# Performance work log

Measured on AMD Instinct MI355X. Metric: run time of the kernel, lower is better.

Reference implementation:

```python
import jax, jax.numpy as jnp
import numpy as np

EPS = 1e-6
NEG_SLOPE = 0.01  # torch LeakyReLU default

def ln(x, g, b):
    m = jnp.mean(x, axis=-1, keepdims=True)
    v = jnp.mean((x - m) ** 2, axis=-1, keepdims=True)
    return (x - m) / jnp.sqrt(v + EPS) * g + b

def leaky(x):
    return jnp.where(x >= 0, x, NEG_SLOPE * x)

def setup_inputs() -> dict:
    B, L, F, H, NH, LBL = 8, 1024, 1024, 256, 8, 4766
    key = jax.random.key(0)
    ks = jax.random.split(key, 16)
    def lin(k, i, o, s=0.03):
        kw, kb = jax.random.split(k)
        return jax.random.normal(kw, (i, o), jnp.float32) * s, jnp.zeros((o,), jnp.float32)
    w_in, b_in = lin(ks[0], F, H)
    w_h, b_h = lin(ks[1], H, H)
    a_w1, a_b1 = lin(ks[2], H, 64)
    a_w2, a_b2 = lin(ks[3], 64, NH)
    o_w1, o_b1 = lin(ks[4], NH * H, NH * H)
    o_w2, o_b2 = lin(ks[5], NH * H, LBL)
    CM = (jax.random.uniform(ks[6], (LBL, LBL)) < 0.002).astype(jnp.float32)
    CM = jnp.maximum(CM, jnp.eye(LBL, dtype=jnp.float32))
    return {
        'h_V': jax.random.normal(ks[7], (B, L, F), jnp.float32),
        'mask': jnp.ones((B, L), jnp.int32),
        'ln0_g': jnp.ones((F,), jnp.float32), 'ln0_b': jnp.zeros((F,), jnp.float32),
        'w_in': w_in, 'b_in': b_in,
        'ln1_g': jnp.ones((H,), jnp.float32), 'ln1_b': jnp.zeros((H,), jnp.float32),
        'w_h': w_h, 'b_h': b_h,
        'ln2_g': jnp.ones((H,), jnp.float32), 'ln2_b': jnp.zeros((H,), jnp.float32),
        'a_w1': a_w1, 'a_b1': a_b1,
        'a_lng': jnp.ones((64,), jnp.float32), 'a_lnb': jnp.zeros((64,), jnp.float32),
        'a_w2': a_w2, 'a_b2': a_b2,
        'o_w1': o_w1, 'o_b1': o_b1,
        'o_lng': jnp.ones((NH * H,), jnp.float32), 'o_lnb': jnp.zeros((NH * H,), jnp.float32),
        'o_w2': o_w2, 'o_b2': o_b2,
        'CM': CM,
    }

def reference(h_V, mask, ln0_g, ln0_b, w_in, b_in, ln1_g, ln1_b, w_h, b_h,
              ln2_g, ln2_b, a_w1, a_b1, a_lng, a_lnb, a_w2, a_b2,
              o_w1, o_b1, o_lng, o_lnb, o_w2, o_b2, CM):
    B = h_V.shape[0]
    # input + hidden blocks (eval mode: dropout is identity)
    x = ln(h_V, ln0_g, ln0_b)
    x = leaky(x @ w_in + b_in)
    x = ln(x, ln1_g, ln1_b)
    x = leaky(x @ w_h + b_h)
    x = ln(x, ln2_g, ln2_b)                      # [B,L,H]
    # multi-head attention pooling over sequence
    a = leaky(x @ a_w1 + a_b1)
    a = ln(a, a_lng, a_lnb)
    a = a @ a_w2 + a_b2                          # [B,L,NH]
    a = jnp.where(mask[:, :, None] == 0, jnp.float32(-1e9), a)
    a = jax.nn.softmax(a, axis=1)
    h = jnp.einsum('blh,bld->bhd', a, x).reshape(B, -1)  # [B,NH*H]
    # output block
    h = leaky(h @ o_w1 + o_b1)
    h = ln(h, o_lng, o_lnb)
    p = jax.nn.sigmoid(h @ o_w2 + o_b2)          # [B,LBL]
    # GO-hierarchy max-product propagation (eval path)
    out = jnp.max(p[:, None, :] * CM[None, :, :], axis=-1)  # [B,LBL]
    return out.astype(jnp.float32)
```

## Files before the change

### kernel.cpp

```cpp
#include <hip/hip_runtime.h>
#include <hip/hip_bf16.h>
#include <cstdint>

#define B_   8
#define L_   1024
#define F_   1024
#define H_   256
#define NH_  8
#define LBL_ 4766
#define M_   (B_*L_)
#define OD_  (NH_*H_)
#define NCM  (LBL_*LBL_)
#define MP_EPB 16384
#define MP_NB  ((NCM + MP_EPB - 1) / MP_EPB)

typedef unsigned short u16;
typedef unsigned int   u32;
typedef __attribute__((ext_vector_type(8))) short short8;
typedef __attribute__((ext_vector_type(4))) float float4v;

#define BF16_ONES_PAIR 0x3f803f80u

__device__ __forceinline__ float bf2f(u32 u) { return __uint_as_float(u << 16); }
__device__ __forceinline__ u16 f2bf(float f) {
    u32 u = __float_as_uint(f);
    u32 r = 0x7fffu + ((u >> 16) & 1u);
    return (u16)((u + r) >> 16);
}

struct f8 { float v[8]; };

__device__ __forceinline__ float ldS(const void* p, size_t i, bool bf) {
    return bf ? bf2f(((const u16*)p)[i]) : ((const float*)p)[i];
}
__device__ __forceinline__ float4 ld4(const void* p, size_t i, bool bf) {
    if (bf) {
        uint2 u = *(const uint2*)((const u16*)p + i);
        return make_float4(bf2f(u.x & 0xffff), bf2f(u.x >> 16),
                           bf2f(u.y & 0xffff), bf2f(u.y >> 16));
    }
    return *(const float4*)((const float*)p + i);
}
__device__ __forceinline__ f8 ld8(const void* p, size_t i, bool bf) {
    f8 r;
    if (bf) {
        uint4 u = *(const uint4*)((const u16*)p + i);
        r.v[0]=bf2f(u.x&0xffff); r.v[1]=bf2f(u.x>>16);
        r.v[2]=bf2f(u.y&0xffff); r.v[3]=bf2f(u.y>>16);
        r.v[4]=bf2f(u.z&0xffff); r.v[5]=bf2f(u.z>>16);
        r.v[6]=bf2f(u.w&0xffff); r.v[7]=bf2f(u.w>>16);
    } else {
        const float* q = (const float*)p + i;
        float4 a = *(const float4*)q, b = *(const float4*)(q+4);
        r.v[0]=a.x; r.v[1]=a.y; r.v[2]=a.z; r.v[3]=a.w;
        r.v[4]=b.x; r.v[5]=b.y; r.v[6]=b.z; r.v[7]=b.w;
    }
    return r;
}

__device__ __forceinline__ float wave_sum(float v) {
    #pragma unroll
    for (int m = 1; m < 64; m <<= 1) v += __shfl_xor(v, m, 64);
    return v;
}
__device__ __forceinline__ float wave_max(float v) {
    #pragma unroll
    for (int m = 1; m < 64; m <<= 1) v = fmaxf(v, __shfl_xor(v, m, 64));
    return v;
}
__device__ __forceinline__ float blk_sum(float v, float* sh) {
    v = wave_sum(v);
    int w = threadIdx.x >> 6, nw = blockDim.x >> 6;
    if ((threadIdx.x & 63) == 0) sh[w] = v;
    __syncthreads();
    float s = sh[0];
    for (int i = 1; i < nw; ++i) s += sh[i];
    __syncthreads();
    return s;
}
__device__ __forceinline__ float blk_max(float v, float* sh) {
    v = wave_max(v);
    int w = threadIdx.x >> 6, nw = blockDim.x >> 6;
    if ((threadIdx.x & 63) == 0) sh[w] = v;
    __syncthreads();
    float s = sh[0];
    for (int i = 1; i < nw; ++i) s = fmaxf(s, sh[i]);
    __syncthreads();
    return s;
}

__global__ __launch_bounds__(256) void transw_k(const void* __restrict__ W,
        u16* __restrict__ WT, int K, int N, const u32* __restrict__ probe) {
    __shared__ u16 tile[64][65];
    bool bf = (probe[0] == BF16_ONES_PAIR);
    int t = threadIdx.x;
    int kt = blockIdx.x * 64, nt = blockIdx.y * 64;
    int r = t >> 2, cq = (t & 3) * 16;
    #pragma unroll
    for (int j = 0; j < 4; ++j) {
        float4 v = ld4(W, (size_t)(kt + r) * N + nt + cq + j * 4, bf);
        tile[r][cq + j*4 + 0] = f2bf(v.x);
        tile[r][cq + j*4 + 1] = f2bf(v.y);
        tile[r][cq + j*4 + 2] = f2bf(v.z);
        tile[r][cq + j*4 + 3] = f2bf(v.w);
    }
    __syncthreads();
    #pragma unroll
    for (int j = 0; j < 4; ++j) {
        int k = cq + j * 4;
        u32 a0 = tile[k+0][r], a1 = tile[k+1][r], a2 = tile[k+2][r], a3 = tile[k+3][r];
        uint2 o; o.x = a0 | (a1 << 16); o.y = a2 | (a3 << 16);
        *(uint2*)(WT + (size_t)(nt + r) * K + kt + k) = o;
    }
}

__global__ __launch_bounds__(256) void lnwrite_k(const void* __restrict__ hv,
        const void* __restrict__ g, const void* __restrict__ b,
        u16* __restrict__ x0, const u32* __restrict__ probe) {
    __shared__ float sh[4];
    bool bf = (probe[0] == BF16_ONES_PAIR);
    int row = blockIdx.x, t = threadIdx.x;
    float4 v = ld4(hv, (size_t)row * F_ + t * 4, bf);
    float s = v.x + v.y + v.z + v.w;
    float q = v.x*v.x + v.y*v.y + v.z*v.z + v.w*v.w;
    s = blk_sum(s, sh);
    q = blk_sum(q, sh);
    float mean = s * (1.f / F_);
    float rstd = rsqrtf(q * (1.f / F_) - mean * mean + 1e-6f);
    float4 gg = ld4(g, t * 4, bf);
    float4 bb = ld4(b, t * 4, bf);
    u32 o0 = f2bf((v.x - mean) * rstd * gg.x + bb.x)
           | ((u32)f2bf((v.y - mean) * rstd * gg.y + bb.y) << 16);
    u32 o1 = f2bf((v.z - mean) * rstd * gg.z + bb.z)
           | ((u32)f2bf((v.w - mean) * rstd * gg.w + bb.w) << 16);
    *(uint2*)(x0 + (size_t)row * F_ + t * 4) = make_uint2(o0, o1);
}

__global__ __launch_bounds__(64) void rowstats_bf_k(const u16* __restrict__ x,
        float2* __restrict__ stat) {
    int row = blockIdx.x, t = threadIdx.x;
    uint2 u = ((const uint2*)(x + (size_t)row * 256))[t];
    float a0 = bf2f(u.x & 0xffff), a1 = bf2f(u.x >> 16);
    float a2 = bf2f(u.y & 0xffff), a3 = bf2f(u.y >> 16);
    float s = wave_sum(a0 + a1 + a2 + a3);
    float q = wave_sum(a0*a0 + a1*a1 + a2*a2 + a3*a3);
    if (t == 0) {
        float m = s * (1.f / 256), v = q * (1.f / 256) - m * m;
        stat[row] = make_float2(m, rsqrtf(v + 1e-6f));
    }
}

__global__ __launch_bounds__(256) void gemm_mfma(const u16* __restrict__ Ap, int amode,
        const float2* __restrict__ stat, const void* __restrict__ g,
        const void* __restrict__ bta, const u16* __restrict__ WT,
        const void* __restrict__ bias, u16* __restrict__ C, int M, int N, int K,
        const u32* __restrict__ probe) {
    __shared__ short8 As[64][5];
    __shared__ short8 Bs[64][5];
    bool pbf = (probe[0] == BF16_ONES_PAIR);
    int t = threadIdx.x;
    int m0 = blockIdx.x * 64, n0 = blockIdx.y * 64;
    int r = t >> 2, kq = t & 3;
    int l = t & 63, w = t >> 6;
    int q = l >> 4, ml = l & 15;
    float4v acc[4];
    #pragma unroll
    for (int nt = 0; nt < 4; ++nt)
        #pragma unroll
        for (int i = 0; i < 4; ++i) acc[nt][i] = 0.f;
    float2 st = (amode == 1) ? stat[m0 + r] : make_float2(0.f, 1.f);
    for (int k0 = 0; k0 < K; k0 += 32) {
        int kk = k0 + kq * 8;
        short8 pa;
        if (amode == 1) {
            f8 a  = ld8(Ap, (size_t)(m0 + r) * K + kk, true);
            f8 gg = ld8(g, kk, pbf);
            f8 bb = ld8(bta, kk, pbf);
            #pragma unroll
            for (int j = 0; j < 8; ++j)
                pa[j] = (short)f2bf((a.v[j] - st.x) * st.y * gg.v[j] + bb.v[j]);
        } else {
            pa = *(const short8*)(Ap + (size_t)(m0 + r) * K + kk);
        }
        short8 pb = *(const short8*)(WT + (size_t)(n0 + r) * K + kk);
        __syncthreads();
        As[r][kq] = pa;
        Bs[r][kq] = pb;
        __syncthreads();
        short8 af = As[w * 16 + ml][q];
        #pragma unroll
        for (int nt = 0; nt < 4; ++nt)
            acc[nt] = __builtin_amdgcn_mfma_f32_16x16x32_bf16(af, Bs[nt*16 + ml][q],
                                                              acc[nt], 0, 0, 0);
    }
    #pragma unroll
    for (int nt = 0; nt < 4; ++nt) {
        int nn = n0 + nt * 16 + ml;
        float bv = ldS(bias, nn, pbf);
        #pragma unroll
        for (int reg = 0; reg < 4; ++reg) {
            float v = acc[nt][reg] + bv;
            v = v >= 0.f ? v : 0.01f * v;
            C[(size_t)(m0 + w * 16 + q * 4 + reg) * N + nn] = f2bf(v);
        }
    }
}

__global__ __launch_bounds__(256) void attnlog_k(const u16* __restrict__ abr,
        const void* __restrict__ g, const void* __restrict__ b,
        const void* __restrict__ w2, const void* __restrict__ b2,
        const int* __restrict__ mask, float* __restrict__ lg,
        const u32* __restrict__ probe) {
    __shared__ float w2s[512];
    __shared__ float b2s[8];
    bool pbf = (probe[0] == BF16_ONES_PAIR);
    int t = threadIdx.x;
    for (int i = t; i < 512; i += 256) w2s[i] = ldS(w2, i, pbf);
    if (t < 8) b2s[t] = ldS(b2, t, pbf);
    __syncthreads();
    int l = t & 63, w = t >> 6;
    int row = blockIdx.x * 4 + w;
    float a = bf2f(abr[(size_t)row * 64 + l]);
    float s = wave_sum(a);
    float q = wave_sum(a * a);
    float m = s * (1.f / 64), var = q * (1.f / 64) - m * m;
    float val = (a - m) * rsqrtf(var + 1e-6f) * ldS(g, l, pbf) + ldS(b, l, pbf);
    float mine = 0.f;
    #pragma unroll
    for (int h = 0; h < 8; ++h) {
        float sh_ = wave_sum(val * w2s[l * 8 + h]);
        if (l == h) mine = sh_;
    }
    if (l < 8) {
        int bb = row >> 10, ll = row & 1023;
        float v = mine + b2s[l];
        if (mask[row] == 0) v = -1e9f;
        lg[((size_t)bb * NH_ + l) * L_ + ll] = v;
    }
}

__global__ __launch_bounds__(256) void softmax2_k(float* __restrict__ lg,
        const float2* __restrict__ st2, float* __restrict__ c1) {
    __shared__ float sh[4];
    int bh = blockIdx.x, t = threadIdx.x;
    int b = bh >> 3;
    size_t base = (size_t)bh * L_;
    float4 v = ((float4*)(lg + base))[t];
    float mx = blk_max(fmaxf(fmaxf(v.x, v.y), fmaxf(v.z, v.w)), sh);
    v.x = expf(v.x - mx); v.y = expf(v.y - mx);
    v.z = expf(v.z - mx); v.w = expf(v.w - mx);
    float s = blk_sum(v.x + v.y + v.z + v.w, sh);
    float inv = 1.f / s;
    float2 s0 = st2[(b << 10) + t*4 + 0];
    float2 s1 = st2[(b << 10) + t*4 + 1];
    float2 s2 = st2[(b << 10) + t*4 + 2];
    float2 s3 = st2[(b << 10) + t*4 + 3];
    float a0 = v.x * inv * s0.y, a1 = v.y * inv * s1.y;
    float a2 = v.z * inv * s2.y, a3 = v.w * inv * s3.y;
    ((float4*)(lg + base))[t] = make_float4(a0, a1, a2, a3);
    float c = blk_sum(a0 * s0.x + a1 * s1.x + a2 * s2.x + a3 * s3.x, sh);
    if (t == 0) c1[bh] = c;
}

__global__ __launch_bounds__(256) void pool_part_k(const float* __restrict__ lg,
        const u16* __restrict__ x2, float* __restrict__ Sp) {
    int bh = blockIdx.x, c = blockIdx.y, t = threadIdx.x;
    int b = bh >> 3, l0 = c << 8;
    const float* aw = lg + (size_t)bh * L_ + l0;
    const u16* xb = x2 + ((size_t)(b << 10) + l0) * 256;
    float acc = 0.f;
    #pragma unroll 4
    for (int i = 0; i < 256; ++i)
        acc += aw[i] * bf2f(xb[(size_t)i * 256 + t]);
    Sp[((size_t)c * 64 + bh) * 256 + t] = acc;
}

__global__ __launch_bounds__(256) void pool_comb_k(const float* __restrict__ Sp,
        const float* __restrict__ c1, const void* __restrict__ g,
        const void* __restrict__ b, float* __restrict__ hp,
        const u32* __restrict__ probe) {
    bool pbf = (probe[0] == BF16_ONES_PAIR);
    int bh = blockIdx.x, t = threadIdx.x;
    float S = Sp[(size_t)bh*256 + t] + Sp[(size_t)(64+bh)*256 + t]
            + Sp[(size_t)(128+bh)*256 + t] + Sp[(size_t)(192+bh)*256 + t];
    hp[(size_t)bh*256 + t] = (S - c1[bh]) * ldS(g, t, pbf) + ldS(b, t, pbf);
}

__global__ __launch_bounds__(256) void gemv2_k(const float* __restrict__ hv,
        const void* __restrict__ W, float* __restrict__ acc, int K, int N,
        const u32* __restrict__ probe) {
    __shared__ float hs[8 * 64];
    bool bf = (probe[0] == BF16_ONES_PAIR);
    int t = threadIdx.x;
    int kb = blockIdx.y * 64;
    for (int i = t; i < 512; i += 256) {
        int r = i >> 6, k = i & 63;
        hs[i] = hv[(size_t)r * K + kb + k];
    }
    __syncthreads();
    int c0 = (blockIdx.x * 256 + t) * 2;
    if (c0 >= N) return;
    float a[8][2] = {};
    #pragma unroll 4
    for (int k = 0; k < 64; ++k) {
        float w0, w1;
        if (bf) {
            u32 u = *(const u32*)((const u16*)W + (size_t)(kb + k) * N + c0);
            w0 = bf2f(u & 0xffff); w1 = bf2f(u >> 16);
        } else {
            float2 fw = *(const float2*)((const float*)W + (size_t)(kb + k) * N + c0);
            w0 = fw.x; w1 = fw.y;
        }
        #pragma unroll
        for (int r = 0; r < 8; ++r) {
            float h = hs[(r << 6) + k];
            a[r][0] += h * w0; a[r][1] += h * w1;
        }
    }
    bool ok1 = (c0 + 1 < N);
    #pragma unroll
    for (int r = 0; r < 8; ++r) {
        atomicAdd(&acc[(size_t)r * N + c0], a[r][0]);
        if (ok1) atomicAdd(&acc[(size_t)r * N + c0 + 1], a[r][1]);
    }
}

__global__ __launch_bounds__(256) void out_ln_k(float* __restrict__ h,
        const void* __restrict__ bias, const void* __restrict__ g,
        const void* __restrict__ b, const u32* __restrict__ probe) {
    __shared__ float sh[4];
    bool bf = (probe[0] == BF16_ONES_PAIR);
    int row = blockIdx.x, t = threadIdx.x;
    float v[8];
    float s = 0.f, q = 0.f;
    #pragma unroll
    for (int i = 0; i < 8; ++i) {
        int c = t + i * 256;
        float x = h[(size_t)row * OD_ + c] + ldS(bias, c, bf);
        x = x >= 0.f ? x : 0.01f * x;
        v[i] = x; s += x; q += x * x;
    }
    s = blk_sum(s, sh) * (1.f / OD_);
    q = blk_sum(q, sh) * (1.f / OD_);
    float rstd = rsqrtf(q - s * s + 1e-6f);
    #pragma unroll
    for (int i = 0; i < 8; ++i) {
        int c = t + i * 256;
        h[(size_t)row * OD_ + c] = (v[i] - s) * rstd * ldS(g, c, bf) + ldS(b, c, bf);
    }
}

__global__ __launch_bounds__(256) void sigmoid_t_k(const float* __restrict__ acc,
        const void* __restrict__ bias, float* __restrict__ pt,
        const u32* __restrict__ probe) {
    bool bf = (probe[0] == BF16_ONES_PAIR);
    int c = blockIdx.x * 256 + threadIdx.x;
    if (c >= LBL_) return;
    float bv = ldS(bias, c, bf);
    float o[8];
    #pragma unroll
    for (int r = 0; r < 8; ++r) {
        float v = acc[(size_t)r * LBL_ + c] + bv;
        o[r] = 1.f / (1.f + expf(-v));
    }
    float4* dst = (float4*)(pt + (size_t)c * 8);
    dst[0] = make_float4(o[0], o[1], o[2], o[3]);
    dst[1] = make_float4(o[4], o[5], o[6], o[7]);
}

__device__ __forceinline__ void mp_hit(u32 idx, float cmv,
        const float* __restrict__ pt, int* smax, u32 rowBase) {
    u32 i = idx / LBL_;
    u32 j = idx - i * LBL_;
    const float4* pj = (const float4*)(pt + (size_t)j * 8);
    float4 pa = pj[0], pb = pj[1];
    int base = (int)(i - rowBase) * 8;
    atomicMax(&smax[base + 0], __float_as_int(pa.x * cmv));
    atomicMax(&smax[base + 1], __float_as_int(pa.y * cmv));
    atomicMax(&smax[base + 2], __float_as_int(pa.z * cmv));
    atomicMax(&smax[base + 3], __float_as_int(pa.w * cmv));
    atomicMax(&smax[base + 4], __float_as_int(pb.x * cmv));
    atomicMax(&smax[base + 5], __float_as_int(pb.y * cmv));
    atomicMax(&smax[base + 6], __float_as_int(pb.z * cmv));
    atomicMax(&smax[base + 7], __float_as_int(pb.w * cmv));
}

__global__ __launch_bounds__(256) void maxprod3_k(const float* __restrict__ pt,
        const void* __restrict__ CM, float* __restrict__ out,
        const u32* __restrict__ probe) {
    __shared__ int smax[6 * 8];
    bool bf = (probe[0] == BF16_ONES_PAIR);
    int t = threadIdx.x;
    size_t blockStart = (size_t)blockIdx.x * MP_EPB;
    u32 rowBase = (u32)(blockStart / LBL_);
    for (int i = t; i < 48; i += 256) smax[i] = 0;
    __syncthreads();
    if (bf) {
        const u16* cm = (const u16*)CM;
        uint4 ch[8];
        size_t i0[8];
        #pragma unroll
        for (int u = 0; u < 8; ++u) {
            size_t idx0 = blockStart + ((size_t)u * 256 + t) * 8;
            i0[u] = idx0;
            ch[u] = (idx0 + 8 <= NCM) ? *(const uint4*)(cm + idx0)
                                      : make_uint4(0, 0, 0, 0);
        }
        #pragma unroll
        for (int u = 0; u < 8; ++u) {
            size_t idx0 = i0[u];
            if (idx0 + 8 <= NCM) {
                uint4 c4 = ch[u];
                if ((c4.x | c4.y | c4.z | c4.w) == 0) continue;
                u32 hw[4] = {c4.x, c4.y, c4.z, c4.w};
                #pragma unroll
                for (int d = 0; d < 4; ++d) {
                    u32 lo = hw[d] & 0xffff, hi = hw[d] >> 16;
                    if (lo) mp_hit((u32)idx0 + d*2,     bf2f(lo), pt, smax, rowBase);
                    if (hi) mp_hit((u32)idx0 + d*2 + 1, bf2f(hi), pt, smax, rowBase);
                }
            } else if (idx0 < NCM) {
                for (u32 e = 0; e < (u32)(NCM - idx0); ++e) {
                    u16 h = cm[idx0 + e];
                    if (h) mp_hit((u32)idx0 + e, bf2f(h), pt, smax, rowBase);
                }
            }
        }
    } else {
        const float* cm = (const float*)CM;
        #pragma unroll
        for (int u = 0; u < 16; ++u) {
            size_t idx0 = blockStart + ((size_t)u * 256 + t) * 4;
            if (idx0 >= NCM) continue;
            float v[4];
            if (idx0 + 4 <= NCM) {
                float4 f = *(const float4*)(cm + idx0);
                v[0] = f.x; v[1] = f.y; v[2] = f.z; v[3] = f.w;
            } else {
                v[0] = v[1] = v[2] = v[3] = 0.f;
                for (u32 e = 0; e < (u32)(NCM - idx0); ++e) v[e] = cm[idx0 + e];
            }
            if (v[0] == 0.f && v[1] == 0.f && v[2] == 0.f && v[3] == 0.f) continue;
            #pragma unroll
            for (int e = 0; e < 4; ++e)
                if (v[e] != 0.f) mp_hit((u32)idx0 + e, v[e], pt, smax, rowBase);
        }
    }
    __syncthreads();
    size_t lastIdx = blockStart + MP_EPB - 1;
    if (lastIdx >= NCM) lastIdx = NCM - 1;
    int nrows = (int)((u32)(lastIdx / LBL_) - rowBase) + 1;
    for (int s = t; s < nrows * 8; s += 256) {
        int v = smax[s];
        if (v != 0) {
            int rr = s >> 3, b = s & 7;
            atomicMax((int*)(out + (size_t)b * LBL_ + rowBase + rr), v);
        }
    }
}

extern "C" void kernel_launch(void* const* d_in, const int* in_sizes, int n_in,
                              void* d_out, int out_size, void* d_ws, size_t ws_size,
                              hipStream_t stream) {
    const void* hv   = d_in[0];
    const int* mask  = (const int*)d_in[1];
    const void* ln0g = d_in[2];
    const void* ln0b = d_in[3];
    const void* w_in = d_in[4];
    const void* b_in = d_in[5];
    const void* ln1g = d_in[6];
    const void* ln1b = d_in[7];
    const void* w_h  = d_in[8];
    const void* b_h  = d_in[9];
    const void* ln2g = d_in[10];
    const void* ln2b = d_in[11];
    const void* aw1  = d_in[12];
    const void* ab1  = d_in[13];
    const void* alng = d_in[14];
    const void* alnb = d_in[15];
    const void* aw2  = d_in[16];
    const void* ab2  = d_in[17];
    const void* ow1  = d_in[18];
    const void* ob1  = d_in[19];
    const void* olng = d_in[20];
    const void* olnb = d_in[21];
    const void* ow2  = d_in[22];
    const void* ob2  = d_in[23];
    const void* CM   = d_in[24];
    const u32* probe = (const u32*)ln0g;
    float* out = (float*)d_out;

    float* f = (float*)d_ws;
    float2* st1 = (float2*)f;
    float2* st2 = st1 + 8192;
    float* lg = f + 2 * 16384;
    float* c1 = lg + 65536;
    float* Sp = c1 + 64;
    float* hp = Sp + 65536;
    float* ha = hp + 16384;
    float* l2 = ha + 16384;
    float* pt = l2 + 38128;
    u16* x0  = (u16*)(pt + 38128);
    u16* x1  = x0 + 8388608;
    u16* x2  = x1 + 2097152;
    u16* abr = x2 + 2097152;
    u16* wt1 = abr + 524288;
    u16* wt2 = wt1 + 262144;
    u16* wt3 = wt2 + 65536;

    hipMemsetAsync(ha, 0, (size_t)(16384 + 38128) * sizeof(float), stream);
    hipMemsetAsync(out, 0, (size_t)(B_ * LBL_) * sizeof(float), stream);

    transw_k<<<dim3(16, 4), 256, 0, stream>>>(w_in, wt1, F_, H_, probe);
    transw_k<<<dim3(4, 4),  256, 0, stream>>>(w_h,  wt2, H_, H_, probe);
    transw_k<<<dim3(4, 1),  256, 0, stream>>>(aw1,  wt3, H_, 64, probe);

    lnwrite_k<<<M_, 256, 0, stream>>>(hv, ln0g, ln0b, x0, probe);
    gemm_mfma<<<dim3(M_/64, 4), 256, 0, stream>>>(x0, 2, nullptr, nullptr, nullptr,
                                                  wt1, b_in, x1, M_, H_, F_, probe);
    rowstats_bf_k<<<M_, 64, 0, stream>>>(x1, st1);
    gemm_mfma<<<dim3(M_/64, 4), 256, 0, stream>>>(x1, 1, st1, ln1g, ln1b,
                                                  wt2, b_h, x2, M_, H_, H_, probe);
    rowstats_bf_k<<<M_, 64, 0, stream>>>(x2, st2);
    gemm_mfma<<<dim3(M_/64, 1), 256, 0, stream>>>(x2, 1, st2, ln2g, ln2b,
                                                  wt3, ab1, abr, M_, 64, H_, probe);

    attnlog_k<<<M_/4, 256, 0, stream>>>(abr, alng, alnb, aw2, ab2, mask, lg, probe);
    softmax2_k<<<B_*NH_, 256, 0, stream>>>(lg, st2, c1);
    pool_part_k<<<dim3(B_*NH_, 4), 256, 0, stream>>>(lg, x2, Sp);
    pool_comb_k<<<B_*NH_, 256, 0, stream>>>(Sp, c1, ln2g, ln2b, hp, probe);

    gemv2_k<<<dim3(OD_/512, 32), 256, 0, stream>>>(hp, ow1, ha, OD_, OD_, probe);
    out_ln_k<<<B_, 256, 0, stream>>>(ha, ob1, olng, olnb, probe);
    gemv2_k<<<dim3((LBL_+511)/512, 32), 256, 0, stream>>>(ha, ow2, l2, OD_, LBL_, probe);
    sigmoid_t_k<<<(LBL_+255)/256, 256, 0, stream>>>(l2, ob2, pt, probe);
    maxprod3_k<<<MP_NB, 256, 0, stream>>>(pt, CM, out, probe);
}
```

Baseline: 385.5 us.

## Fuse prep kernels, compute row stats in GEMM epilogue, merge softmax with pooling

Merges the weight transposes, the input layernorm and the workspace zeroing into one prep kernel. Row mean and variance statistics now come from the GEMM epilogue through shuffles and atomics, replacing the separate rowstats kernels. Softmax and attention pooling become a single kernel per (batch, head), and zeroing the output moves into the sigmoid kernel. This cuts launches, memsets and a re-read of the intermediates, but softpool_k runs only 64 blocks that each walk 1024 rows, which costs parallelism, and the atomic statistics trade some precision (sum/sumsq in fp32).

```diff
diff --git a/kernel.cpp b/kernel.cpp
--- a/kernel.cpp
+++ b/kernel.cpp
@@ -89,16 +89,56 @@
     return s;
 }
 
-__global__ __launch_bounds__(256) void transw_k(const void* __restrict__ W,
-        u16* __restrict__ WT, int K, int N, const u32* __restrict__ probe) {
+__global__ __launch_bounds__(256) void prep_k(const void* __restrict__ hv,
+        const void* __restrict__ g0, const void* __restrict__ b0, u16* __restrict__ x0,
+        const void* __restrict__ w_in, u16* __restrict__ wt1,
+        const void* __restrict__ w_h,  u16* __restrict__ wt2,
+        const void* __restrict__ aw1,  u16* __restrict__ wt3,
+        float* __restrict__ zA, float* __restrict__ zB,
+        const u32* __restrict__ probe) {
     __shared__ u16 tile[64][65];
+    __shared__ float sh[4];
     bool bf = (probe[0] == BF16_ONES_PAIR);
-    int t = threadIdx.x;
-    int kt = blockIdx.x * 64, nt = blockIdx.y * 64;
+    int blk = blockIdx.x, t = threadIdx.x;
+    if (blk < M_) {
+        float4 v = ld4(hv, (size_t)blk * F_ + t * 4, bf);
+        float s = v.x + v.y + v.z + v.w;
+        float q = v.x*v.x + v.y*v.y + v.z*v.z + v.w*v.w;
+        s = blk_sum(s, sh);
+        q = blk_sum(q, sh);
+        float mean = s * (1.f / F_);
+        float rstd = rsqrtf(q * (1.f / F_) - mean * mean + 1e-6f);
+        float4 gg = ld4(g0, t * 4, bf);
+        float4 bb = ld4(b0, t * 4, bf);
+        u32 o0 = f2bf((v.x - mean) * rstd * gg.x + bb.x)
+               | ((u32)f2bf((v.y - mean) * rstd * gg.y + bb.y) << 16);
+        u32 o1 = f2bf((v.z - mean) * rstd * gg.z + bb.z)
+               | ((u32)f2bf((v.w - mean) * rstd * gg.w + bb.w) << 16);
+        *(uint2*)(x0 + (size_t)blk * F_ + t * 4) = make_uint2(o0, o1);
+        return;
+    }
+    blk -= M_;
+    const void* W = nullptr; u16* WT = nullptr; int K = 0, N = 0, kt = 0, nt = 0;
+    if (blk < 64)      { W = w_in; WT = wt1; K = F_; N = H_; kt = blk & 15; nt = blk >> 4; }
+    else if (blk < 80) { int j = blk - 64; W = w_h; WT = wt2; K = H_; N = H_; kt = j & 3; nt = j >> 2; }
+    else if (blk < 84) { int j = blk - 80; W = aw1; WT = wt3; K = H_; N = 64; kt = j; nt = 0; }
+    else {
+        int j = blk - 84;
+        if (j < 16) {
+            float4* p = (float4*)zA;
+            for (int i = j * 256 + t; i < 8192; i += 4096) p[i] = make_float4(0,0,0,0);
+        } else {
+            j -= 16;
+            float4* p = (float4*)zB;
+            for (int i = j * 256 + t; i < 13628; i += 4096) p[i] = make_float4(0,0,0,0);
+        }
+        return;
+    }
+    int kt0 = kt * 64, nt0 = nt * 64;
     int r = t >> 2, cq = (t & 3) * 16;
     #pragma unroll
     for (int j = 0; j < 4; ++j) {
-        float4 v = ld4(W, (size_t)(kt + r) * N + nt + cq + j * 4, bf);
+        float4 v = ld4(W, (size_t)(kt0 + r) * N + nt0 + cq + j * 4, bf);
         tile[r][cq + j*4 + 0] = f2bf(v.x);
         tile[r][cq + j*4 + 1] = f2bf(v.y);
         tile[r][cq + j*4 + 2] = f2bf(v.z);
@@ -110,50 +150,15 @@
         int k = cq + j * 4;
         u32 a0 = tile[k+0][r], a1 = tile[k+1][r], a2 = tile[k+2][r], a3 = tile[k+3][r];
         uint2 o; o.x = a0 | (a1 << 16); o.y = a2 | (a3 << 16);
-        *(uint2*)(WT + (size_t)(nt + r) * K + kt + k) = o;
-    }
-}
-
-__global__ __launch_bounds__(256) void lnwrite_k(const void* __restrict__ hv,
-        const void* __restrict__ g, const void* __restrict__ b,
-        u16* __restrict__ x0, const u32* __restrict__ probe) {
-    __shared__ float sh[4];
-    bool bf = (probe[0] == BF16_ONES_PAIR);
-    int row = blockIdx.x, t = threadIdx.x;
-    float4 v = ld4(hv, (size_t)row * F_ + t * 4, bf);
-    float s = v.x + v.y + v.z + v.w;
-    float q = v.x*v.x + v.y*v.y + v.z*v.z + v.w*v.w;
-    s = blk_sum(s, sh);
-    q = blk_sum(q, sh);
-    float mean = s * (1.f / F_);
-    float rstd = rsqrtf(q * (1.f / F_) - mean * mean + 1e-6f);
-    float4 gg = ld4(g, t * 4, bf);
-    float4 bb = ld4(b, t * 4, bf);
-    u32 o0 = f2bf((v.x - mean) * rstd * gg.x + bb.x)
-           | ((u32)f2bf((v.y - mean) * rstd * gg.y + bb.y) << 16);
-    u32 o1 = f2bf((v.z - mean) * rstd * gg.z + bb.z)
-           | ((u32)f2bf((v.w - mean) * rstd * gg.w + bb.w) << 16);
-    *(uint2*)(x0 + (size_t)row * F_ + t * 4) = make_uint2(o0, o1);
-}
-
-__global__ __launch_bounds__(64) void rowstats_bf_k(const u16* __restrict__ x,
-        float2* __restrict__ stat) {
-    int row = blockIdx.x, t = threadIdx.x;
-    uint2 u = ((const uint2*)(x + (size_t)row * 256))[t];
-    float a0 = bf2f(u.x & 0xffff), a1 = bf2f(u.x >> 16);
-    float a2 = bf2f(u.y & 0xffff), a3 = bf2f(u.y >> 16);
-    float s = wave_sum(a0 + a1 + a2 + a3);
-    float q = wave_sum(a0*a0 + a1*a1 + a2*a2 + a3*a3);
-    if (t == 0) {
-        float m = s * (1.f / 256), v = q * (1.f / 256) - m * m;
-        stat[row] = make_float2(m, rsqrtf(v + 1e-6f));
+        *(uint2*)(WT + (size_t)(nt0 + r) * K + kt0 + k) = o;
     }
 }
 
 __global__ __launch_bounds__(256) void gemm_mfma(const u16* __restrict__ Ap, int amode,
-        const float2* __restrict__ stat, const void* __restrict__ g,
+        const float2* __restrict__ statin, const void* __restrict__ g,
         const void* __restrict__ bta, const u16* __restrict__ WT,
-        const void* __restrict__ bias, u16* __restrict__ C, int M, int N, int K,
+        const void* __restrict__ bias, u16* __restrict__ C,
+        float* __restrict__ statout, int M, int N, int K,
         const u32* __restrict__ probe) {
     __shared__ short8 As[64][5];
     __shared__ short8 Bs[64][5];
@@ -168,7 +173,13 @@
     for (int nt = 0; nt < 4; ++nt)
         #pragma unroll
         for (int i = 0; i < 4; ++i) acc[nt][i] = 0.f;
-    float2 st = (amode == 1) ? stat[m0 + r] : make_float2(0.f, 1.f);
+    float stm = 0.f, str = 1.f;
+    if (amode == 1) {
+        float2 st = statin[m0 + r];
+        float mm = st.x * (1.f / K);
+        stm = mm;
+        str = rsqrtf(st.y * (1.f / K) - mm * mm + 1e-6f);
+    }
     for (int k0 = 0; k0 < K; k0 += 32) {
         int kk = k0 + kq * 8;
         short8 pa;
@@ -178,7 +189,7 @@
             f8 bb = ld8(bta, kk, pbf);
             #pragma unroll
             for (int j = 0; j < 8; ++j)
-                pa[j] = (short)f2bf((a.v[j] - st.x) * st.y * gg.v[j] + bb.v[j]);
+                pa[j] = (short)f2bf((a.v[j] - stm) * str * gg.v[j] + bb.v[j]);
         } else {
             pa = *(const short8*)(Ap + (size_t)(m0 + r) * K + kk);
         }
@@ -193,6 +204,7 @@
             acc[nt] = __builtin_amdgcn_mfma_f32_16x16x32_bf16(af, Bs[nt*16 + ml][q],
                                                               acc[nt], 0, 0, 0);
     }
+    float ov[4][4];
     #pragma unroll
     for (int nt = 0; nt < 4; ++nt) {
         int nn = n0 + nt * 16 + ml;
@@ -201,7 +213,26 @@
         for (int reg = 0; reg < 4; ++reg) {
             float v = acc[nt][reg] + bv;
             v = v >= 0.f ? v : 0.01f * v;
+            ov[nt][reg] = v;
             C[(size_t)(m0 + w * 16 + q * 4 + reg) * N + nn] = f2bf(v);
+        }
+    }
+    if (statout) {
+        #pragma unroll
+        for (int reg = 0; reg < 4; ++reg) {
+            float sv = ov[0][reg] + ov[1][reg] + ov[2][reg] + ov[3][reg];
+            float qv = ov[0][reg]*ov[0][reg] + ov[1][reg]*ov[1][reg]
+                     + ov[2][reg]*ov[2][reg] + ov[3][reg]*ov[3][reg];
+            #pragma unroll
+            for (int mk = 1; mk < 16; mk <<= 1) {
+                sv += __shfl_xor(sv, mk, 64);
+                qv += __shfl_xor(qv, mk, 64);
+            }
+            if (ml == 0) {
+                int row = m0 + w * 16 + q * 4 + reg;
+                atomicAdd(&statout[2 * row],     sv);
+                atomicAdd(&statout[2 * row + 1], qv);
+            }
         }
     }
 }
@@ -239,51 +270,40 @@
     }
 }
 
-__global__ __launch_bounds__(256) void softmax2_k(float* __restrict__ lg,
-        const float2* __restrict__ st2, float* __restrict__ c1) {
+__global__ __launch_bounds__(256) void softpool_k(const float* __restrict__ lg,
+        const float2* __restrict__ st2, const u16* __restrict__ x2,
+        const void* __restrict__ g, const void* __restrict__ b,
+        float* __restrict__ hp, const u32* __restrict__ probe) {
     __shared__ float sh[4];
-    int bh = blockIdx.x, t = threadIdx.x;
-    int b = bh >> 3;
+    __shared__ float awl[1024];
+    bool pbf = (probe[0] == BF16_ONES_PAIR);
+    int bh = blockIdx.x, t = threadIdx.x, bb = bh >> 3;
     size_t base = (size_t)bh * L_;
-    float4 v = ((float4*)(lg + base))[t];
+    float4 v = ((const float4*)(lg + base))[t];
     float mx = blk_max(fmaxf(fmaxf(v.x, v.y), fmaxf(v.z, v.w)), sh);
     v.x = expf(v.x - mx); v.y = expf(v.y - mx);
     v.z = expf(v.z - mx); v.w = expf(v.w - mx);
     float s = blk_sum(v.x + v.y + v.z + v.w, sh);
     float inv = 1.f / s;
-    float2 s0 = st2[(b << 10) + t*4 + 0];
-    float2 s1 = st2[(b << 10) + t*4 + 1];
-    float2 s2 = st2[(b << 10) + t*4 + 2];
-    float2 s3 = st2[(b << 10) + t*4 + 3];
-    float a0 = v.x * inv * s0.y, a1 = v.y * inv * s1.y;
-    float a2 = v.z * inv * s2.y, a3 = v.w * inv * s3.y;
-    ((float4*)(lg + base))[t] = make_float4(a0, a1, a2, a3);
-    float c = blk_sum(a0 * s0.x + a1 * s1.x + a2 * s2.x + a3 * s3.x, sh);
-    if (t == 0) c1[bh] = c;
-}
-
-__global__ __launch_bounds__(256) void pool_part_k(const float* __restrict__ lg,
-        const u16* __restrict__ x2, float* __restrict__ Sp) {
-    int bh = blockIdx.x, c = blockIdx.y, t = threadIdx.x;
-    int b = bh >> 3, l0 = c << 8;
-    const float* aw = lg + (size_t)bh * L_ + l0;
-    const u16* xb = x2 + ((size_t)(b << 10) + l0) * 256;
-    float acc = 0.f;
-    #pragma unroll 4
-    for (int i = 0; i < 256; ++i)
-        acc += aw[i] * bf2f(xb[(size_t)i * 256 + t]);
-    Sp[((size_t)c * 64 + bh) * 256 + t] = acc;
-}
-
-__global__ __launch_bounds__(256) void pool_comb_k(const float* __restrict__ Sp,
-        const float* __restrict__ c1, const void* __restrict__ g,
-        const void* __restrict__ b, float* __restrict__ hp,
-        const u32* __restrict__ probe) {
-    bool pbf = (probe[0] == BF16_ONES_PAIR);
-    int bh = blockIdx.x, t = threadIdx.x;
-    float S = Sp[(size_t)bh*256 + t] + Sp[(size_t)(64+bh)*256 + t]
-            + Sp[(size_t)(128+bh)*256 + t] + Sp[(size_t)(192+bh)*256 + t];
-    hp[(size_t)bh*256 + t] = (S - c1[bh]) * ldS(g, t, pbf) + ldS(b, t, pbf);
+    float va[4] = {v.x, v.y, v.z, v.w};
+    float c1p = 0.f;
+    #pragma unroll
+    for (int j = 0; j < 4; ++j) {
+        int idx = t * 4 + j;
+        float2 st = st2[(bb << 10) + idx];
+        float m = st.x * (1.f / 256);
+        float r = rsqrtf(st.y * (1.f / 256) - m * m + 1e-6f);
+        float aw = va[j] * inv * r;
+        awl[idx] = aw;
+        c1p += aw * m;
+    }
+    float c1 = blk_sum(c1p, sh);
+    const u16* xb = x2 + ((size_t)bb << 10) * 256;
+    float S = 0.f;
+    #pragma unroll 8
+    for (int ll = 0; ll < 1024; ++ll)
+        S += awl[ll] * bf2f(xb[(size_t)ll * 256 + t]);
+    hp[(size_t)bh * 256 + t] = (S - c1) * ldS(g, t, pbf) + ldS(b, t, pbf);
 }
 
 __global__ __launch_bounds__(256) void gemv2_k(const float* __restrict__ hv,
@@ -352,7 +372,7 @@
 
 __global__ __launch_bounds__(256) void sigmoid_t_k(const float* __restrict__ acc,
         const void* __restrict__ bias, float* __restrict__ pt,
-        const u32* __restrict__ probe) {
+        float* __restrict__ out, const u32* __restrict__ probe) {
     bool bf = (probe[0] == BF16_ONES_PAIR);
     int c = blockIdx.x * 256 + threadIdx.x;
     if (c >= LBL_) return;
@@ -362,6 +382,7 @@
     for (int r = 0; r < 8; ++r) {
         float v = acc[(size_t)r * LBL_ + c] + bv;
         o[r] = 1.f / (1.f + expf(-v));
+        out[(size_t)r * LBL_ + c] = 0.f;
     }
     float4* dst = (float4*)(pt + (size_t)c * 8);
     dst[0] = make_float4(o[0], o[1], o[2], o[3]);
@@ -493,10 +514,8 @@
     float* f = (float*)d_ws;
     float2* st1 = (float2*)f;
     float2* st2 = st1 + 8192;
-    float* lg = f + 2 * 16384;
-    float* c1 = lg + 65536;
-    float* Sp = c1 + 64;
-    float* hp = Sp + 65536;
+    float* lg = f + 32768;
+    float* hp = lg + 65536;
     float* ha = hp + 16384;
     float* l2 = ha + 16384;
     float* pt = l2 + 38128;
@@ -508,31 +527,23 @@
     u16* wt2 = wt1 + 262144;
     u16* wt3 = wt2 + 65536;
 
-    hipMemsetAsync(ha, 0, (size_t)(16384 + 38128) * sizeof(float), stream);
-    hipMemsetAsync(out, 0, (size_t)(B_ * LBL_) * sizeof(float), stream);
-
-    transw_k<<<dim3(16, 4), 256, 0, stream>>>(w_in, wt1, F_, H_, probe);
-    transw_k<<<dim3(4, 4),  256, 0, stream>>>(w_h,  wt2, H_, H_, probe);
-    transw_k<<<dim3(4, 1),  256, 0, stream>>>(aw1,  wt3, H_, 64, probe);
-
-    lnwrite_k<<<M_, 256, 0, stream>>>(hv, ln0g, ln0b, x0, probe);
+    prep_k<<<M_ + 84 + 32, 256, 0, stream>>>(hv, ln0g, ln0b, x0,
+                                             w_in, wt1, w_h, wt2, aw1, wt3,
+                                             f, ha, probe);
     gemm_mfma<<<dim3(M_/64, 4), 256, 0, stream>>>(x0, 2, nullptr, nullptr, nullptr,
-                                                  wt1, b_in, x1, M_, H_, F_, probe);
-    rowstats_bf_k<<<M_, 64, 0, stream>>>(x1, st1);
+                                                  wt1, b_in, x1, (float*)st1,
+                                                  M_, H_, F_, probe);
     gemm_mfma<<<dim3(M_/64, 4), 256, 0, stream>>>(x1, 1, st1, ln1g, ln1b,
-                                                  wt2, b_h, x2, M_, H_, H_, probe);
-    rowstats_bf_k<<<M_, 64, 0, stream>>>(x2, st2);
+                                                  wt2, b_h, x2, (float*)st2,
+                                                  M_, H_, H_, probe);
     gemm_mfma<<<dim3(M_/64, 1), 256, 0, stream>>>(x2, 1, st2, ln2g, ln2b,
-                                                  wt3, ab1, abr, M_, 64, H_, probe);
-
+                                                  wt3, ab1, abr, nullptr,
+                                                  M_, 64, H_, probe);
     attnlog_k<<<M_/4, 256, 0, stream>>>(abr, alng, alnb, aw2, ab2, mask, lg, probe);
-    softmax2_k<<<B_*NH_, 256, 0, stream>>>(lg, st2, c1);
-    pool_part_k<<<dim3(B_*NH_, 4), 256, 0, stream>>>(lg, x2, Sp);
-    pool_comb_k<<<B_*NH_, 256, 0, stream>>>(Sp, c1, ln2g, ln2b, hp, probe);
-
+    softpool_k<<<B_*NH_, 256, 0, stream>>>(lg, st2, x2, ln2g, ln2b, hp, probe);
     gemv2_k<<<dim3(OD_/512, 32), 256, 0, stream>>>(hp, ow1, ha, OD_, OD_, probe);
     out_ln_k<<<B_, 256, 0, stream>>>(ha, ob1, olng, olnb, probe);
     gemv2_k<<<dim3((LBL_+511)/512, 32), 256, 0, stream>>>(ha, ow2, l2, OD_, LBL_, probe);
-    sigmoid_t_k<<<(LBL_+255)/256, 256, 0, stream>>>(l2, ob2, pt, probe);
+    sigmoid_t_k<<<(LBL_+255)/256, 256, 0, stream>>>(l2, ob2, pt, out, probe);
     maxprod3_k<<<MP_NB, 256, 0, stream>>>(pt, CM, out, probe);
 }
```

After: 389.4 us. About the same (+1.0%).
